# Kernel optimization log

Hardware: AMD Instinct MI355X
Metric: run time of the kernel (lower is better)

## Reference

```python
import jax, jax.numpy as jnp
import numpy as np

D_MODEL = 1024
D_FF = 2048
N_EXPERTS = 8
TOP_K = 2


def setup_inputs() -> dict:
    key = jax.random.key(0)
    ks = jax.random.split(key, 10)
    s = 0.02
    return {
        "x": jax.random.normal(ks[0], (2, 1024, D_MODEL), dtype=jnp.float32),
        "gate_w": jax.random.normal(ks[1], (N_EXPERTS, D_MODEL), dtype=jnp.float32) * s,
        "gate_b": jnp.zeros((N_EXPERTS,), jnp.float32),
        "Wg": jax.random.normal(ks[2], (N_EXPERTS, D_MODEL, D_FF), dtype=jnp.float32) * s,
        "bg": jnp.zeros((N_EXPERTS, D_FF), jnp.float32),
        "Wu": jax.random.normal(ks[3], (N_EXPERTS, D_MODEL, D_FF), dtype=jnp.float32) * s,
        "bu": jnp.zeros((N_EXPERTS, D_FF), jnp.float32),
        "Wd": jax.random.normal(ks[4], (N_EXPERTS, D_FF, D_MODEL), dtype=jnp.float32) * s,
        "bd": jnp.zeros((N_EXPERTS, D_MODEL), jnp.float32),
    }


def reference(x, gate_w, gate_b, Wg, bg, Wu, bu, Wd, bd):
    b, s, d = x.shape
    xf = x.reshape(-1, d)                       # (T, d)
    T = xf.shape[0]
    # --- router ---
    logits = xf @ gate_w.T + gate_b             # (T, E)
    probs = jax.nn.softmax(logits.astype(jnp.float32), axis=-1)
    # load-balance loss: KL(ideal || mean_probs), reduction='sum'
    expert_probs = probs.mean(axis=0)
    ideal = 1.0 / N_EXPERTS
    balance_loss = jnp.sum(ideal * (jnp.log(ideal) - jnp.log(expert_probs + 1e-9)))
    # top-k routing, renormalized
    vals, idx = jax.lax.top_k(probs, TOP_K)     # (T, K)
    w = vals / vals.sum(axis=-1, keepdims=True)
    # per-token per-expert combine weight (T, E); zero for non-selected experts
    cw = jnp.zeros((T, N_EXPERTS), jnp.float32).at[
        jnp.arange(T)[:, None], idx].add(w)
    # --- experts (SwiGLU MLP), batched over E, masked combine ---
    g = jnp.einsum('td,edf->tef', xf, Wg) + bg[None]   # (T, E, F)
    u = jnp.einsum('td,edf->tef', xf, Wu) + bu[None]
    h = jax.nn.silu(g) * u
    out = jnp.einsum('tef,efd->ted', h, Wd) + bd[None]  # (T, E, d)
    y = jnp.einsum('ted,te->td', out, cw.astype(x.dtype))
    return y.reshape(b, s, d), balance_loss
```

## Files before the change

### kernel.cpp

```cpp
#include <hip/hip_runtime.h>
#include <hip/hip_bf16.h>


#define D_MODEL 1024
#define D_FF    2048
#define N_EXP   8
#define T_TOK   2048
#define MAXTILES 40
#define MAXT64   80

typedef __attribute__((ext_vector_type(8))) short bf16x8;
typedef __attribute__((ext_vector_type(8))) ushort u16x8;
typedef __attribute__((ext_vector_type(4))) float f32x4;

__device__ __forceinline__ ushort f2bf(float f) {
    union { float f; unsigned u; } c; c.f = f;
    unsigned u = c.u;
    return (ushort)((u + 0x7fffu + ((u >> 16) & 1u)) >> 16);
}

__device__ __forceinline__ void glds16(const void* g, void* l) {
    __builtin_amdgcn_global_load_lds(
        (const __attribute__((address_space(1))) unsigned int*)g,
        (__attribute__((address_space(3))) unsigned int*)l, 16, 0, 0);
}

__device__ __forceinline__ void prep_slab_gwu(
    int sp, int tid, const float* __restrict__ Wg, const float* __restrict__ Wu,
    ushort* __restrict__ Wgt, ushort* __restrict__ Wut, ushort* lds)
{
    int which = sp >> 10, s = sp & 1023;
    const float* src = which ? Wu : Wg;
    ushort* dst = which ? Wut : Wgt;
    int e = s >> 7, kt = (s >> 3) & 15, kb = s & 7;
    const float4* p = (const float4*)(src + (size_t)e * 1024 * 2048 + (size_t)(kt * 64 + kb * 8) * 2048);
#pragma unroll
    for (int i = 0; i < 16; i++) {
        float4 v = p[i * 256 + tid];
        ushort4 o;
        o.x = f2bf(v.x); o.y = f2bf(v.y); o.z = f2bf(v.z); o.w = f2bf(v.w);
        *(ushort4*)&lds[(i * 256 + tid) * 4] = o;
    }
    __syncthreads();
    u16x8 in[8];
#pragma unroll
    for (int ko = 0; ko < 8; ko++)
        in[ko] = *(const u16x8*)&lds[ko * 2048 + tid * 8];
    u16x8 out[8];
#pragma unroll
    for (int j = 0; j < 8; j++)
#pragma unroll
        for (int ko = 0; ko < 8; ko++)
            out[j][ko] = in[ko][j];
    __syncthreads();
    int swz = (tid & 7) << 4;
#pragma unroll
    for (int j = 0; j < 8; j++)
        *(u16x8*)((char*)lds + (((8 * tid + j) * 16) ^ swz)) = out[j];
    __syncthreads();
#pragma unroll
    for (int i = 0; i < 8; i++) {
        int c = i * 256 + tid;
        u16x8 v = *(const u16x8*)((char*)lds + ((c * 16) ^ (((c >> 3) & 7) << 4)));
        int R = c >> 7, q = c & 127;
        *(u16x8*)&dst[(size_t)(e * 256 + R * 16 + kt) * 8192 + kb * 1024 + q * 8] = v;
    }
}

__device__ __forceinline__ void prep_slab_wd(
    int s, int tid, const float* __restrict__ Wd, ushort* __restrict__ Wdt, ushort* lds)
{
    int e = s >> 7, kt = (s >> 2) & 31, kbp = s & 3;
    const float4* p = (const float4*)(Wd + (size_t)e * 2048 * 1024 + (size_t)(kt * 64 + kbp * 16) * 1024);
#pragma unroll
    for (int i = 0; i < 16; i++) {
        float4 v = p[i * 256 + tid];
        ushort4 o;
        o.x = f2bf(v.x); o.y = f2bf(v.y); o.z = f2bf(v.z); o.w = f2bf(v.w);
        *(ushort4*)&lds[(i * 256 + tid) * 4] = o;
    }
    __syncthreads();
    u16x8 in[8];
    int th = tid >> 7, tc = tid & 127;
#pragma unroll
    for (int ko = 0; ko < 8; ko++)
        in[ko] = *(const u16x8*)&lds[(th * 8 + ko) * 1024 + tc * 8];
    u16x8 out[8];
#pragma unroll
    for (int j = 0; j < 8; j++)
#pragma unroll
        for (int ko = 0; ko < 8; ko++)
            out[j][ko] = in[ko][j];
    __syncthreads();
    int swz = (tid & 7) << 4;
#pragma unroll
    for (int j = 0; j < 8; j++)
        *(u16x8*)((char*)lds + (((8 * tid + j) * 16) ^ swz)) = out[j];
    __syncthreads();
#pragma unroll
    for (int i = 0; i < 8; i++) {
        int c = i * 256 + tid;
        u16x8 v = *(const u16x8*)((char*)lds + ((c * 16) ^ (((c >> 3) & 7) << 4)));
        int R = c >> 7, q = c & 127;
        int kb2 = R >> 3, ntp = R & 7;
        *(u16x8*)&Wdt[(size_t)(e * 256 + ntp * 32 + kt) * 8192 + (kbp * 2 + kb2) * 1024 + q * 8] = v;
    }
}

union SM1 {
    float gws[N_EXP * D_MODEL];
    ushort prep[16384];
};

__global__ __launch_bounds__(256) void k_router_prep(
    const float* __restrict__ x, const float* __restrict__ gw, const float* __restrict__ gb,
    int* cnt, float* probsum, int* tok, int* slotpk, float* wtok,
    ushort* __restrict__ xb,
    const float* __restrict__ Wg, const float* __restrict__ Wu,
    ushort* __restrict__ Wgt, ushort* __restrict__ Wut)
{
    __shared__ __align__(16) SM1 smem;
    __shared__ float ps_s[N_EXP];
    __shared__ int   bc_s[N_EXP];
    __shared__ int   gb_s[N_EXP];
    __shared__ int   a_e[64];
    __shared__ int   a_lp[64];

    int tid = threadIdx.x;
    int bid = blockIdx.x;

    if (bid >= 64) {
        prep_slab_gwu(bid - 64, tid, Wg, Wu, Wgt, Wut, smem.prep);
        return;
    }

    float* gws = smem.gws;
    for (int i = tid; i < N_EXP * D_MODEL / 4; i += 256)
        ((float4*)gws)[i] = ((const float4*)gw)[i];
    if (tid < N_EXP) { ps_s[tid] = 0.f; bc_s[tid] = 0; }
    __syncthreads();

    int wave = tid >> 6, lane = tid & 63;

    for (int it = 0; it < 8; it++) {
        int tb = it * 4 + wave;
        int t = bid * 32 + tb;
        const float4* xr = (const float4*)(x + (size_t)t * D_MODEL);
        ushort* xbr = xb + (size_t)t * D_MODEL;

        float acc[N_EXP];
#pragma unroll
        for (int e = 0; e < N_EXP; e++) acc[e] = 0.f;
#pragma unroll
        for (int q = 0; q < 4; q++) {
            int idx = q * 64 + lane;
            float4 xv = xr[idx];
            ushort4 xc;
            xc.x = f2bf(xv.x); xc.y = f2bf(xv.y); xc.z = f2bf(xv.z); xc.w = f2bf(xv.w);
            *(ushort4*)&xbr[idx * 4] = xc;
#pragma unroll
            for (int e = 0; e < N_EXP; e++) {
                float4 gv = ((const float4*)(gws + e * D_MODEL))[idx];
                acc[e] += xv.x * gv.x + xv.y * gv.y + xv.z * gv.z + xv.w * gv.w;
            }
        }
#pragma unroll
        for (int off = 32; off > 0; off >>= 1) {
#pragma unroll
            for (int e = 0; e < N_EXP; e++) acc[e] += __shfl_xor(acc[e], off, 64);
        }
        if (lane == 0) {
            float l[N_EXP], m = -1e30f;
#pragma unroll
            for (int e = 0; e < N_EXP; e++) { l[e] = acc[e] + gb[e]; m = fmaxf(m, l[e]); }
            float p[N_EXP], s = 0.f;
#pragma unroll
            for (int e = 0; e < N_EXP; e++) { p[e] = expf(l[e] - m); s += p[e]; }
            float inv = 1.f / s;
#pragma unroll
            for (int e = 0; e < N_EXP; e++) { p[e] *= inv; atomicAdd(&ps_s[e], p[e]); }
            int i0 = 0; float v0 = p[0];
#pragma unroll
            for (int e = 1; e < N_EXP; e++) if (p[e] > v0) { v0 = p[e]; i0 = e; }
            int i1 = -1; float v1 = -1.f;
#pragma unroll
            for (int e = 0; e < N_EXP; e++) if (e != i0 && p[e] > v1) { v1 = p[e]; i1 = e; }
            float winv = 1.f / (v0 + v1);
            int lp0 = atomicAdd(&bc_s[i0], 1);
            int lp1 = atomicAdd(&bc_s[i1], 1);
            a_e[tb * 2 + 0] = i0; a_lp[tb * 2 + 0] = lp0;
            a_e[tb * 2 + 1] = i1; a_lp[tb * 2 + 1] = lp1;
            wtok[t * 2 + 0] = v0 * winv;
            wtok[t * 2 + 1] = v1 * winv;
        }
    }
    __syncthreads();
    if (tid < N_EXP) {
        gb_s[tid] = atomicAdd(&cnt[tid], bc_s[tid]);
        atomicAdd(&probsum[tid], ps_s[tid]);
    }
    __syncthreads();
    if (tid < 64) {
        int tb = tid >> 1, k = tid & 1;
        int t = bid * 32 + tb;
        int e = a_e[tid];
        int slot = gb_s[e] + a_lp[tid];
        tok[e * T_TOK + slot] = t;
        slotpk[t * 2 + k] = (e << 16) | slot;
    }
}

__global__ void k_base_loss(const int* __restrict__ cnt, const float* __restrict__ probsum,
                            int* abase, int* tile, int* tile64, float* loss_out)
{
    if (threadIdx.x == 0 && blockIdx.x == 0) {
        int b = 0, nt = 0, n64 = 0;
        float loss = 0.f;
        for (int e = 0; e < N_EXP; e++) {
            abase[e] = b;
            for (int m0 = 0; m0 < cnt[e]; m0 += 128)
                tile[nt++] = (e << 16) | m0;
            for (int m0 = 0; m0 < cnt[e]; m0 += 64)
                tile64[n64++] = (e << 16) | m0;
            b += ((cnt[e] + 127) >> 7) * 128;
            float mean = probsum[e] * (1.0f / T_TOK);
            loss += 0.125f * (logf(0.125f) - logf(mean + 1e-9f));
        }
        for (; nt < MAXTILES; nt++) tile[nt] = -1;
        for (; n64 < MAXT64; n64++) tile64[n64] = -1;
        *loss_out = loss;
    }
}

struct SM_GU { ushort As[128 * 88]; ushort Bg[8192]; ushort Bu[8192]; };
union SM3 {
    SM_GU g;
    ushort prep[16384];
};

__global__ __launch_bounds__(256, 2) void k_gu_prepwd(
    const ushort* __restrict__ Wgt, const ushort* __restrict__ Wut,
    const float* __restrict__ bg, const float* __restrict__ bu,
    const ushort* __restrict__ xb, const int* __restrict__ cnt,
    const int* __restrict__ abase, const int* __restrict__ tile,
    const int* __restrict__ tok, ushort* __restrict__ h_t,
    const float* __restrict__ Wd, ushort* __restrict__ Wdt)
{
    __shared__ __align__(16) SM3 smem;

    int bid = blockIdx.x;
    int tid = threadIdx.x;

    if (bid >= MAXTILES * 16) {
        prep_slab_wd(bid - MAXTILES * 16, tid, Wd, Wdt, smem.prep);
        return;
    }

    int ti = tile[bid % MAXTILES];
    if (ti < 0) return;
    int e = ti >> 16, m0 = ti & 0xffff;
    int ne = cnt[e];
    int nt = bid / MAXTILES;
    int n0 = nt * 128;
    int stile = (abase[e] >> 7) + (m0 >> 7);

    ushort* As = smem.g.As;
    ushort* Bg_s = smem.g.Bg;
    ushort* Bu_s = smem.g.Bu;

    int lane = tid & 63, wave = tid >> 6;
    int wm = (wave & 1) * 64, wn = (wave >> 1) * 64;

    int arow = tid >> 1;
    int akh = (tid & 1) * 32;
    int atok = tok[e * T_TOK + min(m0 + arow, ne - 1)];
    const ushort* xrow = xb + (size_t)atok * D_MODEL;

    const char* gbase = (const char*)(Wgt + (size_t)(e * 16 + nt) * 16 * 8192);
    const char* ubase = (const char*)(Wut + (size_t)(e * 16 + nt) * 16 * 8192);
    int goff = tid * 16;
    int loff = (tid >> 6) * 1024;

    f32x4 accg[4][4], accu[4][4];
#pragma unroll
    for (int i = 0; i < 4; i++)
#pragma unroll
        for (int j = 0; j < 4; j++) {
            accg[i][j] = (f32x4){0.f, 0.f, 0.f, 0.f};
            accu[i][j] = (f32x4){0.f, 0.f, 0.f, 0.f};
        }

    for (int kt = 0; kt < D_MODEL / 64; kt++) {
        __syncthreads();
#pragma unroll
        for (int q = 0; q < 4; q++)
            *(uint4*)&As[arow * 88 + akh + q * 8] = *(const uint4*)&xrow[kt * 64 + akh + q * 8];
        const char* gsrc = gbase + kt * 16384;
        const char* usrc = ubase + kt * 16384;
#pragma unroll
        for (int q = 0; q < 4; q++) {
            glds16(gsrc + q * 4096 + goff, (char*)Bg_s + q * 4096 + loff);
            glds16(usrc + q * 4096 + goff, (char*)Bu_s + q * 4096 + loff);
        }
        __syncthreads();
#pragma unroll
        for (int ks = 0; ks < 2; ks++) {
            bf16x8 af[4];
            int arow_f = wm + (lane & 15);
            int akb = ks * 32 + (lane >> 4) * 8;
#pragma unroll
            for (int sm_ = 0; sm_ < 4; sm_++)
                af[sm_] = *(const bf16x8*)&As[(arow_f + sm_ * 16) * 88 + akb];
            int bkb = ks * 4 + (lane >> 4);
#pragma unroll
            for (int sn = 0; sn < 4; sn++) {
                int ncol = wn + sn * 16 + (lane & 15);
                bf16x8 bgf = *(const bf16x8*)&Bg_s[(bkb * 128 + ncol) * 8];
                bf16x8 buf = *(const bf16x8*)&Bu_s[(bkb * 128 + ncol) * 8];
#pragma unroll
                for (int sm_ = 0; sm_ < 4; sm_++) {
                    accg[sm_][sn] = __builtin_amdgcn_mfma_f32_16x16x32_bf16(af[sm_], bgf, accg[sm_][sn], 0, 0, 0);
                    accu[sm_][sn] = __builtin_amdgcn_mfma_f32_16x16x32_bf16(af[sm_], buf, accu[sm_][sn], 0, 0, 0);
                }
            }
        }
    }
    int rbase = wm + ((lane >> 4) << 2);
    int cbase = wn + (lane & 15);
    size_t tbase = (size_t)stile * 32 * 8192;
#pragma unroll
    for (int sm_ = 0; sm_ < 4; sm_++) {
#pragma unroll
        for (int r = 0; r < 4; r++) {
            int pos = m0 + rbase + sm_ * 16 + r;
            if (pos < ne) {
                int row = pos & 127;
#pragma unroll
                for (int sn = 0; sn < 4; sn++) {
                    int col = n0 + cbase + sn * 16;
                    float g = accg[sm_][sn][r] + bg[e * D_FF + col];
                    float u = accu[sm_][sn][r] + bu[e * D_FF + col];
                    float hv = (g / (1.f + expf(-g))) * u;
                    int ktb = col >> 6, kb = (col >> 3) & 7, ko = col & 7;
                    h_t[tbase + (size_t)ktb * 8192 + (kb * 128 + row) * 8 + ko] = f2bf(hv);
                }
            }
        }
    }
}

__global__ __launch_bounds__(256, 2) void k_expert_down(
    const ushort* __restrict__ Wdt, const float* __restrict__ bd,
    const ushort* __restrict__ h_t, const int* __restrict__ cnt,
    const int* __restrict__ abase, const int* __restrict__ tile64,
    float* __restrict__ outp)
{
    int ti = tile64[blockIdx.x];
    if (ti < 0) return;
    int e = ti >> 16, m0 = ti & 0xffff;
    int ne = cnt[e];
    int nt = blockIdx.y;
    int n0 = nt * 128;
    int stile = (abase[e] >> 7) + (m0 >> 7);
    int hoff = (m0 & 64) ? 1024 : 0;

    __shared__ __align__(16) ushort As8[4096];
    __shared__ __align__(16) ushort Bd_s[8192];

    int tid = threadIdx.x;
    int lane = tid & 63, wave = tid >> 6;
    int wm = (wave & 1) * 32, wn = (wave >> 1) * 64;

    const char* hbase = (const char*)(h_t + (size_t)stile * 32 * 8192);
    const char* dbase = (const char*)(Wdt + (size_t)(e * 8 + nt) * 32 * 8192);
    int goff = tid * 16;
    int loff = (tid >> 6) * 1024;

    f32x4 acc[2][4];
#pragma unroll
    for (int i = 0; i < 2; i++)
#pragma unroll
        for (int j = 0; j < 4; j++) acc[i][j] = (f32x4){0.f, 0.f, 0.f, 0.f};

    for (int kt = 0; kt < D_FF / 64; kt++) {
        __syncthreads();
#pragma unroll
        for (int q = 0; q < 2; q++) {
            int c = q * 256 + tid;
            int kb = c >> 6;
            glds16(hbase + kt * 16384 + kb * 2048 + hoff + (c & 63) * 16,
                   (char*)As8 + q * 4096 + loff);
        }
        const char* bsrc = dbase + kt * 16384;
#pragma unroll
        for (int q = 0; q < 4; q++)
            glds16(bsrc + q * 4096 + goff, (char*)Bd_s + q * 4096 + loff);
        __syncthreads();
#pragma unroll
        for (int ks = 0; ks < 2; ks++) {
            int kb = ks * 4 + (lane >> 4);
            int arow_l = wm + (lane & 15);
            bf16x8 af[2];
#pragma unroll
            for (int sm_ = 0; sm_ < 2; sm_++)
                af[sm_] = *(const bf16x8*)&As8[(kb * 64 + arow_l + sm_ * 16) * 8];
#pragma unroll
            for (int sn = 0; sn < 4; sn++) {
                int ncol = wn + sn * 16 + (lane & 15);
                bf16x8 bdf = *(const bf16x8*)&Bd_s[(kb * 128 + ncol) * 8];
#pragma unroll
                for (int sm_ = 0; sm_ < 2; sm_++)
                    acc[sm_][sn] = __builtin_amdgcn_mfma_f32_16x16x32_bf16(af[sm_], bdf, acc[sm_][sn], 0, 0, 0);
            }
        }
    }
    int rbase = wm + ((lane >> 4) << 2);
    int cbase = wn + (lane & 15);
#pragma unroll
    for (int sm_ = 0; sm_ < 2; sm_++) {
#pragma unroll
        for (int r = 0; r < 4; r++) {
            int pos = m0 + rbase + sm_ * 16 + r;
            if (pos < ne) {
                size_t ob = (size_t)(abase[e] + pos) * D_MODEL;
#pragma unroll
                for (int sn = 0; sn < 4; sn++) {
                    int col = n0 + cbase + sn * 16;
                    outp[ob + col] = acc[sm_][sn][r] + bd[e * D_MODEL + col];
                }
            }
        }
    }
}

__global__ void k_combine(const float* __restrict__ outp, const int* __restrict__ slotpk,
                          const float* __restrict__ wtok, const int* __restrict__ abase,
                          float* __restrict__ y)
{
    int idx = blockIdx.x * 256 + threadIdx.x;
    int t = idx >> 8, j = idx & 255;
    int sp0 = slotpk[t * 2 + 0], sp1 = slotpk[t * 2 + 1];
    float w0 = wtok[t * 2 + 0], w1 = wtok[t * 2 + 1];
    size_t s0 = (size_t)abase[sp0 >> 16] + (sp0 & 0xffff);
    size_t s1 = (size_t)abase[sp1 >> 16] + (sp1 & 0xffff);
    float4 a = ((const float4*)outp)[s0 * (D_MODEL / 4) + j];
    float4 b = ((const float4*)outp)[s1 * (D_MODEL / 4) + j];
    float4 o;
    o.x = w0 * a.x + w1 * b.x;
    o.y = w0 * a.y + w1 * b.y;
    o.z = w0 * a.z + w1 * b.z;
    o.w = w0 * a.w + w1 * b.w;
    ((float4*)y)[idx] = o;
}

extern "C" void kernel_launch(void* const* d_in, const int* in_sizes, int n_in,
                              void* d_out, int out_size, void* d_ws, size_t ws_size,
                              hipStream_t stream)
{
    const float* x  = (const float*)d_in[0];
    const float* gw = (const float*)d_in[1];
    const float* gb = (const float*)d_in[2];
    const float* Wg = (const float*)d_in[3];
    const float* bg = (const float*)d_in[4];
    const float* Wu = (const float*)d_in[5];
    const float* bu = (const float*)d_in[6];
    const float* Wd = (const float*)d_in[7];
    const float* bd = (const float*)d_in[8];
    float* y = (float*)d_out;
    float* loss_out = y + (size_t)T_TOK * D_MODEL;

    char* ws = (char*)d_ws;
    int*    cnt     = (int*)(ws + 0);
    float*  probsum = (float*)(ws + 128);
    int*    abase   = (int*)(ws + 256);
    int*    tiletab = (int*)(ws + 320);
    int*    slotpk  = (int*)(ws + 512);
    float*  wtok    = (float*)(ws + 16896);
    int*    tok     = (int*)(ws + 33280);
    int*    tile64  = (int*)(ws + 98816);
    ushort* xb      = (ushort*)(ws + 131072);
    ushort* Wgt     = (ushort*)(ws + 4325376);
    ushort* Wut     = (ushort*)(ws + 37879808);
    ushort* Wdt     = (ushort*)(ws + 71434240);
    ushort* h_t     = (ushort*)(ws + 104988672);
    float*  outp    = (float*)(ws + 125960192);

    (void)hipMemsetAsync(d_ws, 0, 256, stream);
    k_router_prep<<<dim3(64 + 2048), dim3(256), 0, stream>>>(
        x, gw, gb, cnt, probsum, tok, slotpk, wtok, xb, Wg, Wu, Wgt, Wut);
    k_base_loss<<<dim3(1), dim3(64), 0, stream>>>(cnt, probsum, abase, tiletab, tile64, loss_out);
    k_gu_prepwd<<<dim3(MAXTILES * 16 + 1024), dim3(256), 0, stream>>>(
        Wgt, Wut, bg, bu, xb, cnt, abase, tiletab, tok, h_t, Wd, Wdt);
    k_expert_down<<<dim3(MAXT64, 8), dim3(256), 0, stream>>>(
        Wdt, bd, h_t, cnt, abase, tile64, outp);
    k_combine<<<dim3(2048), dim3(256), 0, stream>>>(outp, slotpk, wtok, abase, y);
}
```

Measured before the change: 350.9 us.

## Double-buffer gate/up weight tiles and prefetch activations with swizzled LDS layout

Splits the gate/up B tiles into two LDS buffers and issues the global-to-LDS loads for the next K step before computing the current one, with explicit waitcnt and barriers in place of the two syncthreads per iteration. The next A row chunk is prefetched into registers, and the A tile moves from a padded stride to an XOR-swizzled 64-wide layout to avoid bank conflicts. The aim is to hide global load latency behind MFMA work. LDS use grows to roughly 80KB per block, which may cut occupancy below the two blocks per CU requested by the launch bounds, and the hand-written vmcnt counts have to match the number of loads in flight.

```diff
diff --git a/kernel.cpp b/kernel.cpp
--- a/kernel.cpp
+++ b/kernel.cpp
@@ -232,7 +232,11 @@
     }
 }
 
-struct SM_GU { ushort As[128 * 88]; ushort Bg[8192]; ushort Bu[8192]; };
+struct SM_GU {
+    ushort As[8192];
+    ushort Bg0[8192], Bg1[8192];
+    ushort Bu0[8192], Bu1[8192];
+};
 union SM3 {
     SM_GU g;
     ushort prep[16384];
@@ -264,9 +268,9 @@
     int n0 = nt * 128;
     int stile = (abase[e] >> 7) + (m0 >> 7);
 
-    ushort* As = smem.g.As;
-    ushort* Bg_s = smem.g.Bg;
-    ushort* Bu_s = smem.g.Bu;
+    ushort* As   = smem.g.As;
+    ushort* Bg0  = smem.g.Bg0; ushort* Bg1 = smem.g.Bg1;
+    ushort* Bu0  = smem.g.Bu0; ushort* Bu1 = smem.g.Bu1;
 
     int lane = tid & 63, wave = tid >> 6;
     int wm = (wave & 1) * 64, wn = (wave >> 1) * 64;
@@ -275,6 +279,12 @@
     int akh = (tid & 1) * 32;
     int atok = tok[e * T_TOK + min(m0 + arow, ne - 1)];
     const ushort* xrow = xb + (size_t)atok * D_MODEL;
+    int adst[4];
+#pragma unroll
+    for (int q = 0; q < 4; q++) {
+        int koct = (tid & 1) * 4 + q;
+        adst[q] = arow * 64 + ((koct ^ (arow & 7)) * 8);
+    }
 
     const char* gbase = (const char*)(Wgt + (size_t)(e * 16 + nt) * 16 * 8192);
     const char* ubase = (const char*)(Wut + (size_t)(e * 16 + nt) * 16 * 8192);
@@ -290,33 +300,56 @@
             accu[i][j] = (f32x4){0.f, 0.f, 0.f, 0.f};
         }
 
-    for (int kt = 0; kt < D_MODEL / 64; kt++) {
-        __syncthreads();
+    uint4 a_regs[4];
+#pragma unroll
+    for (int q = 0; q < 4; q++)
+        a_regs[q] = *(const uint4*)&xrow[akh + q * 8];
+#pragma unroll
+    for (int q = 0; q < 4; q++) {
+        glds16(gbase + q * 4096 + goff, (char*)Bg0 + q * 4096 + loff);
+        glds16(ubase + q * 4096 + goff, (char*)Bu0 + q * 4096 + loff);
+    }
+
+    ushort* Bgc = Bg0; ushort* Bgn = Bg1;
+    ushort* Buc = Bu0; ushort* Bun = Bu1;
+
+    for (int kt = 0; kt < 16; kt++) {
 #pragma unroll
         for (int q = 0; q < 4; q++)
-            *(uint4*)&As[arow * 88 + akh + q * 8] = *(const uint4*)&xrow[kt * 64 + akh + q * 8];
-        const char* gsrc = gbase + kt * 16384;
-        const char* usrc = ubase + kt * 16384;
-#pragma unroll
-        for (int q = 0; q < 4; q++) {
-            glds16(gsrc + q * 4096 + goff, (char*)Bg_s + q * 4096 + loff);
-            glds16(usrc + q * 4096 + goff, (char*)Bu_s + q * 4096 + loff);
-        }
-        __syncthreads();
+            *(uint4*)&As[adst[q]] = a_regs[q];
+        if (kt < 15) {
+#pragma unroll
+            for (int q = 0; q < 4; q++)
+                a_regs[q] = *(const uint4*)&xrow[(kt + 1) * 64 + akh + q * 8];
+            const char* gsrc = gbase + (kt + 1) * 16384;
+            const char* usrc = ubase + (kt + 1) * 16384;
+#pragma unroll
+            for (int q = 0; q < 4; q++) {
+                glds16(gsrc + q * 4096 + goff, (char*)Bgn + q * 4096 + loff);
+                glds16(usrc + q * 4096 + goff, (char*)Bun + q * 4096 + loff);
+            }
+            asm volatile("s_waitcnt vmcnt(12) lgkmcnt(0)" ::: "memory");
+        } else {
+            asm volatile("s_waitcnt vmcnt(0) lgkmcnt(0)" ::: "memory");
+        }
+        __builtin_amdgcn_s_barrier();
+        __builtin_amdgcn_sched_barrier(0);
 #pragma unroll
         for (int ks = 0; ks < 2; ks++) {
             bf16x8 af[4];
-            int arow_f = wm + (lane & 15);
-            int akb = ks * 32 + (lane >> 4) * 8;
-#pragma unroll
-            for (int sm_ = 0; sm_ < 4; sm_++)
-                af[sm_] = *(const bf16x8*)&As[(arow_f + sm_ * 16) * 88 + akb];
+            int r0 = wm + (lane & 15);
+            int koct = ks * 4 + (lane >> 4);
+#pragma unroll
+            for (int sm_ = 0; sm_ < 4; sm_++) {
+                int r = r0 + sm_ * 16;
+                af[sm_] = *(const bf16x8*)&As[r * 64 + ((koct ^ (r & 7)) * 8)];
+            }
             int bkb = ks * 4 + (lane >> 4);
 #pragma unroll
             for (int sn = 0; sn < 4; sn++) {
                 int ncol = wn + sn * 16 + (lane & 15);
-                bf16x8 bgf = *(const bf16x8*)&Bg_s[(bkb * 128 + ncol) * 8];
-                bf16x8 buf = *(const bf16x8*)&Bu_s[(bkb * 128 + ncol) * 8];
+                bf16x8 bgf = *(const bf16x8*)&Bgc[(bkb * 128 + ncol) * 8];
+                bf16x8 buf = *(const bf16x8*)&Buc[(bkb * 128 + ncol) * 8];
 #pragma unroll
                 for (int sm_ = 0; sm_ < 4; sm_++) {
                     accg[sm_][sn] = __builtin_amdgcn_mfma_f32_16x16x32_bf16(af[sm_], bgf, accg[sm_][sn], 0, 0, 0);
@@ -324,7 +357,11 @@
                 }
             }
         }
-    }
+        if (kt < 15) __builtin_amdgcn_s_barrier();
+        ushort* t1 = Bgc; Bgc = Bgn; Bgn = t1;
+        ushort* t2 = Buc; Buc = Bun; Bun = t2;
+    }
+
     int rbase = wm + ((lane >> 4) << 2);
     int cbase = wn + (lane & 15);
     size_t tbase = (size_t)stile * 32 * 8192;
```

Result: slower. 385.8 us (+9.9%).
